# Performance work log

Measured on AMD Instinct MI355X. Metric: run time of the kernel, lower is better.

The kernel has to match this reference:

```python
import jax, jax.numpy as jnp
import numpy as np

N, F, T, C, E = 5000, 4, 12, 600, 160000


def setup_inputs() -> dict:
    key = jax.random.key(0)
    ks = jax.random.split(key, 18)
    x = jax.random.normal(ks[0], (N, F, T), jnp.float32)
    edge_index = jax.random.randint(ks[1], (2, E), 0, N)
    edge_attributes = jax.random.uniform(ks[2], (E,), jnp.float32)
    s_in = 0.5   # glorot-ish scale for F->C conv weights
    s_lin = 0.03  # scale for (2C)->C gate linears
    return {
        "x": x,
        "edge_index": edge_index,
        "edge_attributes": edge_attributes,
        # GCNConv weights/biases for z, r, h gates (weight stored [F, C])
        "W_z": jax.random.normal(ks[3], (F, C), jnp.float32) * s_in,
        "b_z": jnp.zeros((C,), jnp.float32),
        "W_r": jax.random.normal(ks[4], (F, C), jnp.float32) * s_in,
        "b_r": jnp.zeros((C,), jnp.float32),
        "W_h": jax.random.normal(ks[5], (F, C), jnp.float32) * s_in,
        "b_h": jnp.zeros((C,), jnp.float32),
        # gate Linear(2C, C) weights in torch layout [out=C, in=2C]
        "Wlz": jax.random.normal(ks[6], (C, 2 * C), jnp.float32) * s_lin,
        "blz": jnp.zeros((C,), jnp.float32),
        "Wlr": jax.random.normal(ks[7], (C, 2 * C), jnp.float32) * s_lin,
        "blr": jnp.zeros((C,), jnp.float32),
        "Wlh": jax.random.normal(ks[8], (C, 2 * C), jnp.float32) * s_lin,
        "blh": jnp.zeros((C,), jnp.float32),
        # temporal attention logits over periods
        "att": jax.random.normal(ks[9], (T,), jnp.float32),
        # head Linear(600, periods), torch layout [T, C]
        "W_head": jax.random.normal(ks[10], (T, C), jnp.float32) * 0.04,
        "b_head": jnp.zeros((T,), jnp.float32),
    }


def _gcn_propagate(x, edge_index, edge_weight):
    """A_hat @ x with A_hat = D^{-1/2}(A+I)D^{-1/2} (GCNConv norm, self-loops w=1).
    x: [N, F, T] -> [N, F, T]."""
    loop = jnp.arange(N)
    row = jnp.concatenate([edge_index[0], loop])   # source j
    col = jnp.concatenate([edge_index[1], loop])   # target i
    w = jnp.concatenate([edge_weight, jnp.ones((N,), x.dtype)])
    deg = jax.ops.segment_sum(w, col, num_segments=N)
    dis = jnp.where(deg > 0, jax.lax.rsqrt(deg), 0.0)
    norm = dis[row] * w * dis[col]                 # [E+N]
    msgs = norm[:, None, None] * x[row]            # gather + scale, [E+N, F, T]
    return jax.ops.segment_sum(msgs, col, num_segments=N)


def reference(x, edge_index, edge_attributes,
              W_z, b_z, W_r, b_r, W_h, b_h,
              Wlz, blz, Wlr, blr, Wlh, blh,
              att, W_head, b_head):
    # A3TGCN: H is passed as None each period -> zeros, never threaded across
    # time. Hence z*H == 0 and the H*r candidate term == 0 exactly; the r-gate
    # (W_r, b_r, Wlr, blr) and the second halves of Wlz/Wlh drop out of the math.
    agg = _gcn_propagate(x, edge_index, edge_attributes)          # [N, F, T]
    # GCNConv output = A_hat X W + b (linear commutes with propagation)
    conv_z = jnp.einsum('nft,fc->nct', agg, W_z) + b_z[:, None]   # [N, C, T]
    conv_h = jnp.einsum('nft,fc->nct', agg, W_h) + b_h[:, None]
    # gate linears on cat([conv, H]) with H = 0 -> only first C input columns
    z = jax.nn.sigmoid(jnp.einsum('nct,dc->ndt', conv_z, Wlz[:, :C]) + blz[:, None])
    h_tilde = jnp.tanh(jnp.einsum('nct,dc->ndt', conv_h, Wlh[:, :C]) + blh[:, None])
    H_t = (1.0 - z) * h_tilde                                      # z*H = 0
    probs = jax.nn.softmax(att)                                    # [T]
    H_accum = jnp.einsum('nct,t->nc', H_t, probs)                  # [N, C]
    return jax.nn.relu(H_accum) @ W_head.T + b_head                # [N, T]
```

## Files before the change

kernel.cpp:

```cpp
#include <hip/hip_runtime.h>

#define NN 5000
#define NF 4
#define NT 12
#define NC 600
#define NCP 640
#define NE 160000
#define FT 48
#define LOG2E 1.4426950408889634f

typedef float v2f __attribute__((ext_vector_type(2)));


__global__ void k_init(int* __restrict__ cnt, float* __restrict__ tabG) {
    int i = blockIdx.x * blockDim.x + threadIdx.x;
    if (i < 5000) cnt[i] = 0;
    else if (i < 19092) tabG[i - 5000] = 0.f;
}

#define CNT_BLOCKS 625
#define WB_WAVES 6132
__global__ __launch_bounds__(256) void k_count(
        const int* __restrict__ ei,
        int* __restrict__ cnt, int* __restrict__ rank,
        const float* __restrict__ Wz, const float* __restrict__ bz,
        const float* __restrict__ Wh, const float* __restrict__ bh,
        const float* __restrict__ Wlz, const float* __restrict__ blz,
        const float* __restrict__ Wlh, const float* __restrict__ blh,
        const float* __restrict__ att, const float* __restrict__ Whead,
        float* __restrict__ tabG) {
    int bid = blockIdx.x;
    int tid = threadIdx.x;
    if (bid < CNT_BLOCKS) {
        int e = bid * 256 + tid;
        if (e < NE) rank[e] = atomicAdd(&cnt[ei[NE + e]], 1);
        return;
    }
    int wid = (bid - CNT_BLOCKS) * 4 + (tid >> 6);
    int lane = tid & 63;
    if (wid >= WB_WAVES) return;

    if (wid < 6000) {
        const float* va;
        const float* vb;
        float scale, bias = 0.f;
        if (wid < 2400) {
            int f = wid / NC, d = wid % NC;
            va = Wz + f * NC; vb = Wlz + d * (2 * NC); scale = LOG2E;
        } else if (wid < 4800) {
            int j = wid - 2400;
            int f = j / NC, d = j % NC;
            va = Wh + f * NC; vb = Wlh + d * (2 * NC); scale = 2.0f * LOG2E;
        } else if (wid < 5400) {
            int d = wid - 4800;
            va = bz; vb = Wlz + d * (2 * NC); scale = LOG2E; bias = blz[d];
        } else {
            int d = wid - 5400;
            va = bh; vb = Wlh + d * (2 * NC); scale = 2.0f * LOG2E; bias = blh[d];
        }
        float s = 0.f;
        for (int c = lane; c < NC; c += 64) s = fmaf(va[c], vb[c], s);
#pragma unroll
        for (int off = 32; off > 0; off >>= 1) s += __shfl_down(s, off, 64);
        if (lane == 0) {
            float r = scale * (bias + s);
            if (wid < 2400) {
                int f = wid / NC, d = wid % NC;
                tabG[d * 4 + f] = r;
            } else if (wid < 4800) {
                int j = wid - 2400;
                int f = j / NC, d = j % NC;
                tabG[2560 + d * 4 + f] = r;
            } else if (wid < 5400) {
                tabG[5120 + (wid - 4800) * 2] = r;
            } else {
                tabG[5120 + (wid - 5400) * 2 + 1] = r;
            }
        }
    } else if (wid < 6012) {
        if (lane == 0) {
            int t = wid - 6000;
            float m = att[0];
            for (int k = 1; k < NT; ++k) m = fmaxf(m, att[k]);
            float ssum = 0.f;
            for (int k = 0; k < NT; ++k) ssum += __expf(att[k] - m);
            tabG[14080 + t] = __expf(att[t] - m) / ssum;
        }
    } else {
        int i = (wid - 6012) * 64 + lane;
        if (i < 7680) {
            int j = i & 3;
            int rest = i >> 2;
            int d = rest % NCP, q = rest / NCP;
            float v = (d < NC) ? Whead[(4 * q + j) * NC + d] : 0.f;
            tabG[6400 + i] = v;
        }
    }
}

#define SCAN_CHUNK 20
__global__ __launch_bounds__(256) void k_scan(const int* __restrict__ cnt,
                                              int* __restrict__ base) {
    __shared__ int part[256];
    int t = threadIdx.x;
    int start = t * SCAN_CHUNK;
    int s = 0;
#pragma unroll
    for (int k = 0; k < SCAN_CHUNK; ++k) {
        int idx = start + k;
        if (idx < NN) s += cnt[idx];
    }
    part[t] = s;
    __syncthreads();
    for (int off = 1; off < 256; off <<= 1) {
        int v = (t >= off) ? part[t - off] : 0;
        __syncthreads();
        part[t] += v;
        __syncthreads();
    }
    int running = (t == 0) ? 0 : part[t - 1];
#pragma unroll
    for (int k = 0; k < SCAN_CHUNK; ++k) {
        int idx = start + k;
        if (idx < NN) {
            base[idx] = running;
            running += cnt[idx];
        }
    }
    if (t == 255) base[NN] = part[255];
}

__global__ void k_scatter(const int* __restrict__ ei, const float* __restrict__ w,
                          const int* __restrict__ base, const int* __restrict__ rank,
                          int2* __restrict__ epak) {
    int e = blockIdx.x * blockDim.x + threadIdx.x;
    if (e < NE) {
        int2 p; p.x = ei[e]; p.y = __float_as_int(w[e]);
        epak[base[ei[NE + e]] + rank[e]] = p;
    }
}

__global__ __launch_bounds__(64) void k_deg_dis(const int2* __restrict__ epak,
                                                const int* __restrict__ base,
                                                float* __restrict__ dis) {
    int n = blockIdx.x;
    int lane = threadIdx.x;
    int b0 = base[n], b1 = base[n + 1];
    float s = 0.f;
    for (int j = b0 + lane; j < b1; j += 64) s += __int_as_float(epak[j].y);
#pragma unroll
    for (int off = 32; off > 0; off >>= 1) s += __shfl_down(s, off, 64);
    if (lane == 0) dis[n] = rsqrtf(1.0f + s);
}

__global__ __launch_bounds__(64) void k_gather(
        const float* __restrict__ x, const float* __restrict__ dis,
        const int2* __restrict__ epak, const int* __restrict__ base,
        float* __restrict__ agg) {
    int n = blockIdx.x;
    int lane = threadIdx.x;
    int b0 = base[n], b1 = base[n + 1];
    float dn = dis[n];
    float acc = 0.f;
    if (lane < FT) acc = dn * x[n * FT + lane];
    int j = b0;
    for (; j + 3 < b1; j += 4) {
        int2 p0 = epak[j], p1 = epak[j + 1], p2 = epak[j + 2], p3 = epak[j + 3];
        float n0 = dis[p0.x] * __int_as_float(p0.y);
        float n1 = dis[p1.x] * __int_as_float(p1.y);
        float n2 = dis[p2.x] * __int_as_float(p2.y);
        float n3 = dis[p3.x] * __int_as_float(p3.y);
        if (lane < FT) {
            acc += n0 * x[p0.x * FT + lane];
            acc += n1 * x[p1.x * FT + lane];
            acc += n2 * x[p2.x * FT + lane];
            acc += n3 * x[p3.x * FT + lane];
        }
    }
    for (; j < b1; ++j) {
        int2 p0 = epak[j];
        float n0 = dis[p0.x] * __int_as_float(p0.y);
        if (lane < FT) acc += n0 * x[p0.x * FT + lane];
    }
    if (lane < FT) agg[n * FT + lane] = dn * acc;
}

__global__ __launch_bounds__(256, 4) void k_main(
        const float* __restrict__ agg, const float* __restrict__ tabG,
        const float* __restrict__ bhead, float* __restrict__ out) {
    __shared__ float red[4][NT][16];
    int tid = threadIdx.x;
    int wid = __builtin_amdgcn_readfirstlane(tid >> 6);
    int lane = tid & 63;
    int n = blockIdx.x * 4 + wid;

    const float4* mz4 = (const float4*)tabG;
    const float4* mh4 = (const float4*)(tabG + 2560);
    const float2* bzh = (const float2*)(tabG + 5120);
    const float4* wt4 = (const float4*)(tabG + 6400);

    const v2f* ag2 = (const v2f*)(agg + n * FT);
    v2f A2[24];
#pragma unroll
    for (int i = 0; i < 24; ++i) A2[i] = ag2[i];

    v2f pp[6];
#pragma unroll
    for (int tp = 0; tp < 6; ++tp) { pp[tp].x = tabG[14080 + 2 * tp]; pp[tp].y = tabG[14080 + 2 * tp + 1]; }

    float outp[NT];
#pragma unroll
    for (int t = 0; t < NT; ++t) outp[t] = 0.f;

#pragma unroll
    for (int it = 0; it < 10; ++it) {
        int dd = it * 64 + lane;

        float4 mzv = mz4[dd];
        float4 mhv = mh4[dd];
        float2 bb = bzh[dd];

        v2f hacc; hacc.x = 0.f; hacc.y = 0.f;
#pragma unroll
        for (int tp = 0; tp < 6; ++tp) {
            v2f u; u.x = bb.x; u.y = bb.x;
            v2f v; v.x = bb.y; v.y = bb.y;
            u += A2[0 * 6 + tp] * mzv.x;
            u += A2[1 * 6 + tp] * mzv.y;
            u += A2[2 * 6 + tp] * mzv.z;
            u += A2[3 * 6 + tp] * mzv.w;
            v += A2[0 * 6 + tp] * mhv.x;
            v += A2[1 * 6 + tp] * mhv.y;
            v += A2[2 * 6 + tp] * mhv.z;
            v += A2[3 * 6 + tp] * mhv.w;
            v2f eu; eu.x = exp2f(u.x); eu.y = exp2f(u.y);
            v2f ev; ev.x = exp2f(v.x); ev.y = exp2f(v.y);
            v2f den = (eu + 1.f) * (ev + 1.f);
            v2f rd; rd.x = __builtin_amdgcn_rcpf(den.x); rd.y = __builtin_amdgcn_rcpf(den.y);
            v2f num = pp[tp] * (ev - 1.f);
            hacc += num * rd;
        }
        float r = fmaxf(hacc.x + hacc.y, 0.f);

        float4 w0 = wt4[0 * NCP + dd], w1 = wt4[1 * NCP + dd], w2 = wt4[2 * NCP + dd];
        outp[0]  = fmaf(r, w0.x, outp[0]);   outp[1]  = fmaf(r, w0.y, outp[1]);
        outp[2]  = fmaf(r, w0.z, outp[2]);   outp[3]  = fmaf(r, w0.w, outp[3]);
        outp[4]  = fmaf(r, w1.x, outp[4]);   outp[5]  = fmaf(r, w1.y, outp[5]);
        outp[6]  = fmaf(r, w1.z, outp[6]);   outp[7]  = fmaf(r, w1.w, outp[7]);
        outp[8]  = fmaf(r, w2.x, outp[8]);   outp[9]  = fmaf(r, w2.y, outp[9]);
        outp[10] = fmaf(r, w2.z, outp[10]);  outp[11] = fmaf(r, w2.w, outp[11]);
    }

#pragma unroll
    for (int t = 0; t < NT; ++t) {
        float v = outp[t];
        v += __shfl_xor(v, 32, 64);
        v += __shfl_xor(v, 16, 64);
        if (lane < 16) red[wid][t][lane] = v;
    }
    if (lane < NT) {
        const float4* row = (const float4*)red[wid][lane];
        float4 a = row[0], b = row[1], c = row[2], d = row[3];
        float s = ((a.x + a.y) + (a.z + a.w)) + ((b.x + b.y) + (b.z + b.w))
                + ((c.x + c.y) + (c.z + c.w)) + ((d.x + d.y) + (d.z + d.w));
        out[n * NT + lane] = s + bhead[lane];
    }
}

extern "C" void kernel_launch(void* const* d_in, const int* in_sizes, int n_in,
                              void* d_out, int out_size, void* d_ws, size_t ws_size,
                              hipStream_t stream) {
    const float* x     = (const float*)d_in[0];
    const int*   ei    = (const int*)d_in[1];
    const float* ea    = (const float*)d_in[2];
    const float* Wz    = (const float*)d_in[3];
    const float* bz    = (const float*)d_in[4];
    const float* Wh    = (const float*)d_in[7];
    const float* bh    = (const float*)d_in[8];
    const float* Wlz   = (const float*)d_in[9];
    const float* blz   = (const float*)d_in[10];
    const float* Wlh   = (const float*)d_in[13];
    const float* blh   = (const float*)d_in[14];
    const float* att   = (const float*)d_in[15];
    const float* Whead = (const float*)d_in[16];
    const float* bhead = (const float*)d_in[17];
    float* out = (float*)d_out;

    float* ws   = (float*)d_ws;
    int*   cnt  = (int*)ws;
    int*   base = (int*)(ws + 5000);
    int*   rank = (int*)(ws + 10008);
    int2*  epak = (int2*)(ws + 170008);
    float* dis  = ws + 490008;
    float* agg  = ws + 495008;
    float* tabG = ws + 735008;

    k_init<<<(19092 + 255) / 256, 256, 0, stream>>>(cnt, tabG);
    k_count<<<CNT_BLOCKS + (WB_WAVES + 3) / 4, 256, 0, stream>>>(
        ei, cnt, rank,
        Wz, bz, Wh, bh, Wlz, blz, Wlh, blh, att, Whead, tabG);
    k_scan<<<1, 256, 0, stream>>>(cnt, base);
    k_scatter<<<(NE + 255) / 256, 256, 0, stream>>>(ei, ea, base, rank, epak);
    k_deg_dis<<<NN, 64, 0, stream>>>(epak, base, dis);
    k_gather<<<NN, 64, 0, stream>>>(x, dis, epak, base, agg);
    k_main<<<NN / 4, 256, 0, stream>>>(agg, tabG, bhead, out);
}
```

Measured before the change: 76.52 us.

## Pack edge count and fixed-point degree into one 64-bit atomic, drop deg kernel

Each edge now does a single 64-bit atomicAdd that carries the in-degree count in the upper 20 bits and the edge weight, as 26-bit fixed point, in the lower 44 bits. The scan kernel reads the packed value to produce both the CSR base and dis = rsqrt(1+deg). This removes the separate k_deg_dis launch and its extra pass over epak. In exchange the degree sum is quantized to fixed point, which introduces a small rounding error, and the atomics are 64-bit instead of 32-bit.

```diff
diff --git a/kernel.cpp b/kernel.cpp
--- a/kernel.cpp
+++ b/kernel.cpp
@@ -8,21 +8,24 @@
 #define NE 160000
 #define FT 48
 #define LOG2E 1.4426950408889634f
+#define WSCALE 67108864.0f
+#define MASK44 ((1ULL << 44) - 1)
 
 typedef float v2f __attribute__((ext_vector_type(2)));
-
-
-__global__ void k_init(int* __restrict__ cnt, float* __restrict__ tabG) {
+typedef unsigned long long u64;
+
+
+__global__ void k_init(int* __restrict__ cnt64, float* __restrict__ tabG) {
     int i = blockIdx.x * blockDim.x + threadIdx.x;
-    if (i < 5000) cnt[i] = 0;
-    else if (i < 19092) tabG[i - 5000] = 0.f;
+    if (i < 10000) cnt64[i] = 0;
+    else if (i < 24092) tabG[i - 10000] = 0.f;
 }
 
 #define CNT_BLOCKS 625
 #define WB_WAVES 6132
 __global__ __launch_bounds__(256) void k_count(
-        const int* __restrict__ ei,
-        int* __restrict__ cnt, int* __restrict__ rank,
+        const int* __restrict__ ei, const float* __restrict__ w,
+        u64* __restrict__ cnt64, int* __restrict__ rank,
         const float* __restrict__ Wz, const float* __restrict__ bz,
         const float* __restrict__ Wh, const float* __restrict__ bh,
         const float* __restrict__ Wlz, const float* __restrict__ blz,
@@ -33,7 +36,12 @@
     int tid = threadIdx.x;
     if (bid < CNT_BLOCKS) {
         int e = bid * 256 + tid;
-        if (e < NE) rank[e] = atomicAdd(&cnt[ei[NE + e]], 1);
+        if (e < NE) {
+            int c = ei[NE + e];
+            u64 fixed = (u64)(w[e] * WSCALE + 0.5f);
+            u64 old = atomicAdd(&cnt64[c], (1ULL << 44) | fixed);
+            rank[e] = (int)(old >> 44);
+        }
         return;
     }
     int wid = (bid - CNT_BLOCKS) * 4 + (tid >> 6);
@@ -99,8 +107,9 @@
 }
 
 #define SCAN_CHUNK 20
-__global__ __launch_bounds__(256) void k_scan(const int* __restrict__ cnt,
-                                              int* __restrict__ base) {
+__global__ __launch_bounds__(256) void k_scan(const u64* __restrict__ cnt64,
+                                              int* __restrict__ base,
+                                              float* __restrict__ dis) {
     __shared__ int part[256];
     int t = threadIdx.x;
     int start = t * SCAN_CHUNK;
@@ -108,7 +117,7 @@
 #pragma unroll
     for (int k = 0; k < SCAN_CHUNK; ++k) {
         int idx = start + k;
-        if (idx < NN) s += cnt[idx];
+        if (idx < NN) s += (int)(cnt64[idx] >> 44);
     }
     part[t] = s;
     __syncthreads();
@@ -123,8 +132,11 @@
     for (int k = 0; k < SCAN_CHUNK; ++k) {
         int idx = start + k;
         if (idx < NN) {
+            u64 v = cnt64[idx];
             base[idx] = running;
-            running += cnt[idx];
+            running += (int)(v >> 44);
+            float deg = (float)(v & MASK44) * (1.0f / WSCALE);
+            dis[idx] = rsqrtf(1.0f + deg);
         }
     }
     if (t == 255) base[NN] = part[255];
@@ -138,19 +150,6 @@
         int2 p; p.x = ei[e]; p.y = __float_as_int(w[e]);
         epak[base[ei[NE + e]] + rank[e]] = p;
     }
-}
-
-__global__ __launch_bounds__(64) void k_deg_dis(const int2* __restrict__ epak,
-                                                const int* __restrict__ base,
-                                                float* __restrict__ dis) {
-    int n = blockIdx.x;
-    int lane = threadIdx.x;
-    int b0 = base[n], b1 = base[n + 1];
-    float s = 0.f;
-    for (int j = b0 + lane; j < b1; j += 64) s += __int_as_float(epak[j].y);
-#pragma unroll
-    for (int off = 32; off > 0; off >>= 1) s += __shfl_down(s, off, 64);
-    if (lane == 0) dis[n] = rsqrtf(1.0f + s);
 }
 
 __global__ __launch_bounds__(64) void k_gather(
@@ -286,22 +285,21 @@
     const float* bhead = (const float*)d_in[17];
     float* out = (float*)d_out;
 
-    float* ws   = (float*)d_ws;
-    int*   cnt  = (int*)ws;
-    int*   base = (int*)(ws + 5000);
-    int*   rank = (int*)(ws + 10008);
-    int2*  epak = (int2*)(ws + 170008);
-    float* dis  = ws + 490008;
-    float* agg  = ws + 495008;
-    float* tabG = ws + 735008;
-
-    k_init<<<(19092 + 255) / 256, 256, 0, stream>>>(cnt, tabG);
+    float* ws    = (float*)d_ws;
+    u64*   cnt64 = (u64*)ws;
+    int*   base  = (int*)(ws + 10000);
+    int*   rank  = (int*)(ws + 15008);
+    int2*  epak  = (int2*)(ws + 175008);
+    float* dis   = ws + 495008;
+    float* agg   = ws + 500008;
+    float* tabG  = ws + 740008;
+
+    k_init<<<(24092 + 255) / 256, 256, 0, stream>>>((int*)cnt64, tabG);
     k_count<<<CNT_BLOCKS + (WB_WAVES + 3) / 4, 256, 0, stream>>>(
-        ei, cnt, rank,
+        ei, ea, cnt64, rank,
         Wz, bz, Wh, bh, Wlz, blz, Wlh, blh, att, Whead, tabG);
-    k_scan<<<1, 256, 0, stream>>>(cnt, base);
+    k_scan<<<1, 256, 0, stream>>>(cnt64, base, dis);
     k_scatter<<<(NE + 255) / 256, 256, 0, stream>>>(ei, ea, base, rank, epak);
-    k_deg_dis<<<NN, 64, 0, stream>>>(epak, base, dis);
     k_gather<<<NN, 64, 0, stream>>>(x, dis, epak, base, agg);
     k_main<<<NN / 4, 256, 0, stream>>>(agg, tabG, bhead, out);
 }
```

New measurement: 81.48 us. +6.5%, slower.
